# Kernel tuning notes

Measured on AMD Instinct MI355X. Metric: run time of the kernel, lower is better.

Reference implementation:

```python
import jax, jax.numpy as jnp
import numpy as np

B, C, H, W = 16, 128, 128, 128


def _gram(feat):
    # feat: [B, C, H, W] -> [B, C, HW]; gram: [B, C, C]
    f = feat.reshape(feat.shape[0], feat.shape[1], -1)
    return jnp.einsum('bcn,bdn->bcd', f, f)


def setup_inputs() -> dict:
    key = jax.random.key(0)
    k1, k2 = jax.random.split(key)
    feat = jax.random.normal(k1, (B, C, H, W), dtype=jnp.float32)
    feat_decod = jax.random.normal(k2, (B, C, H, W), dtype=jnp.float32)
    return {"feat": feat, "feat_decod": feat_decod}


def reference(feat, feat_decod):
    feat_size = feat.shape[2] * feat.shape[3]  # H*W
    feat_nb = feat.shape[1]                     # C
    gram_enc = _gram(feat)
    gram_dec = _gram(feat_decod)
    diff = gram_dec - gram_enc
    # per-sample scalar loss: [B]
    denom = 4.0 * feat_size * feat_size * feat_nb * feat_nb
    return jnp.sum(diff * diff, axis=(-2, -1)) / denom
```

## Files before the change

### kernel.cpp

```cpp
#include <hip/hip_runtime.h>
#include <hip/hip_bf16.h>


typedef __attribute__((ext_vector_type(8))) short short8;
typedef __attribute__((ext_vector_type(4))) float f32x4;

#define CC 128
#define NN 16384

__device__ __forceinline__ short f2bf(float x) {
    unsigned u = __builtin_bit_cast(unsigned, x);
    u += 0x7fffu + ((u >> 16) & 1u);
    return (short)(u >> 16);
}

__global__ __launch_bounds__(256, 4) void gram_partial_k(
    const float* __restrict__ f0, const float* __restrict__ f1,
    float* __restrict__ partials, int S, int Kc, int nst)
{
    __shared__ short lds[2][CC * 64];

    const int tid = threadIdx.x;
    const int bx  = blockIdx.x;
    const int g   = bx & 31;
    const int s   = bx >> 5;

    const float* src  = (g & 1) ? f1 : f0;
    const float* base = src + (size_t)(g >> 1) * ((size_t)CC * NN) + (size_t)s * Kc;

    const int srow = tid >> 3;
    const int scb  = tid & 7;
    const float* gp = base + (size_t)srow * NN + scb * 8;

    const int lane = tid & 63;
    const int w    = tid >> 6;
    const int m0   = (w & 1) * 64;
    const int n0   = (w >> 1) * 64;
    const int lr   = lane & 15;
    const int lk   = lane >> 4;

    const int rot = bx & (nst - 1);

    f32x4 acc[4][4];
    #pragma unroll
    for (int i = 0; i < 4; ++i)
        #pragma unroll
        for (int j = 0; j < 4; ++j)
            acc[i][j] = (f32x4){0.f, 0.f, 0.f, 0.f};

    float4 ra[4], rb[4];

    auto load_stage = [&](int st) {
        int sp = (st + rot) & (nst - 1);
        #pragma unroll
        for (int it = 0; it < 4; ++it) {
            const float* p = gp + (size_t)it * 32 * NN + (size_t)sp * 64;
            ra[it] = *(const float4*)p;
            rb[it] = *(const float4*)(p + 4);
        }
    };

    auto store_stage = [&](int buf) {
        #pragma unroll
        for (int it = 0; it < 4; ++it) {
            int r = srow + 32 * it;
            short8 v = { f2bf(ra[it].x), f2bf(ra[it].y), f2bf(ra[it].z), f2bf(ra[it].w),
                         f2bf(rb[it].x), f2bf(rb[it].y), f2bf(rb[it].z), f2bf(rb[it].w) };
            int phys = scb ^ (r & 7);
            *(short8*)&lds[buf][r * 64 + phys * 8] = v;
        }
    };

    auto compute = [&](int buf) {
        #pragma unroll
        for (int ks = 0; ks < 2; ++ks) {
            short8 af[4], bfr[4];
            int cb = ks * 4 + lk;
            #pragma unroll
            for (int i = 0; i < 4; ++i) {
                int r = m0 + i * 16 + lr;
                af[i] = *(const short8*)&lds[buf][r * 64 + ((cb ^ (r & 7)) * 8)];
            }
            #pragma unroll
            for (int i = 0; i < 4; ++i) {
                int r = n0 + i * 16 + lr;
                bfr[i] = *(const short8*)&lds[buf][r * 64 + ((cb ^ (r & 7)) * 8)];
            }
            #pragma unroll
            for (int mi = 0; mi < 4; ++mi)
                #pragma unroll
                for (int ni = 0; ni < 4; ++ni)
                    acc[mi][ni] = __builtin_amdgcn_mfma_f32_16x16x32_bf16(
                        af[mi], bfr[ni], acc[mi][ni], 0, 0, 0);
        }
    };

    load_stage(0);
    store_stage(0);
    __syncthreads();
    for (int st = 0; st < nst; ++st) {
        int cur = st & 1;
        bool more = (st + 1 < nst);
        if (more) load_stage(st + 1);
        compute(cur);
        if (more) store_stage(cur ^ 1);
        __syncthreads();
    }

    float* op = partials + ((size_t)g * S + s) * (CC * CC);
    #pragma unroll
    for (int mi = 0; mi < 4; ++mi)
        #pragma unroll
        for (int ni = 0; ni < 4; ++ni)
            #pragma unroll
            for (int i = 0; i < 4; ++i) {
                int row = m0 + mi * 16 + lk * 4 + i;
                int col = n0 + ni * 16 + lr;
                op[row * CC + col] = acc[mi][ni][i];
            }
}

__global__ __launch_bounds__(256) void reduce1_k(
    const float* __restrict__ partials, float* __restrict__ part2, int S)
{
    int b     = blockIdx.x >> 4;
    int chunk = blockIdx.x & 15;
    int t     = threadIdx.x;
    size_t e  = (size_t)chunk * 1024 + (size_t)t * 4;

    const f32x4* Pe = (const f32x4*)(partials + ((size_t)(2 * b) * S) * (CC * CC) + e);
    const f32x4* Pd = (const f32x4*)(partials + ((size_t)(2 * b + 1) * S) * (CC * CC) + e);
    const size_t stride = (size_t)CC * CC / 4;

    f32x4 ae = {0.f, 0.f, 0.f, 0.f}, ad = {0.f, 0.f, 0.f, 0.f};
    #pragma unroll 8
    for (int s2 = 0; s2 < S; ++s2) {
        ae += Pe[(size_t)s2 * stride];
        ad += Pd[(size_t)s2 * stride];
    }
    f32x4 d = ad - ae;
    float v = d[0] * d[0] + d[1] * d[1] + d[2] * d[2] + d[3] * d[3];
    #pragma unroll
    for (int off = 32; off > 0; off >>= 1) v += __shfl_down(v, off);
    __shared__ float wsum[4];
    if ((t & 63) == 0) wsum[t >> 6] = v;
    __syncthreads();
    if (t == 0) part2[b * 16 + chunk] = wsum[0] + wsum[1] + wsum[2] + wsum[3];
}

__global__ void reduce2_k(const float* __restrict__ part2, float* __restrict__ out)
{
    int b = blockIdx.x;
    int t = threadIdx.x;
    float v = (t < 16) ? part2[b * 16 + t] : 0.f;
    #pragma unroll
    for (int off = 8; off > 0; off >>= 1) v += __shfl_down(v, off);
    if (t == 0) out[b] = v * (1.0f / 17592186044416.0f);
}

extern "C" void kernel_launch(void* const* d_in, const int* in_sizes, int n_in,
                              void* d_out, int out_size, void* d_ws, size_t ws_size,
                              hipStream_t stream)
{
    const float* f0 = (const float*)d_in[0];
    const float* f1 = (const float*)d_in[1];
    float* out = (float*)d_out;

    const size_t perS = 32ull * CC * CC * 4;
    const size_t tail = 16 * 16 * 4;
    int S = 32;
    while (S > 1 && perS * (size_t)S + tail > ws_size) S >>= 1;
    int Kc  = NN / S;
    int nst = Kc / 64;

    float* partials = (float*)d_ws;
    float* part2    = (float*)((char*)d_ws + perS * (size_t)S);

    gram_partial_k<<<32 * S, 256, 0, stream>>>(f0, f1, partials, S, Kc, nst);
    reduce1_k<<<16 * 16, 256, 0, stream>>>(partials, part2, S);
    reduce2_k<<<16, 64, 0, stream>>>(part2, out);
}
```

Before: 299.1 us.

## Pre-pack inputs to swizzled bf16 tiles and stream them via global_load_lds

Adds a pack kernel that converts both fp32 feature tensors into bf16 stage tiles already laid out in the swizzled LDS format. The gram kernel then copies those tiles straight into LDS with global_load_lds, which removes the per-stage register conversion and the LDS store work. The split count drops from 32 to 16 and occupancy hints change. The cost is an extra pass that writes and re-reads 128 MB of packed data. A fallback direct kernel runs when the workspace is too small.

```diff
diff --git a/kernel.cpp b/kernel.cpp
--- a/kernel.cpp
+++ b/kernel.cpp
@@ -1,8 +1,8 @@
 #include <hip/hip_runtime.h>
-#include <hip/hip_bf16.h>
 
 
 typedef __attribute__((ext_vector_type(8))) short short8;
+typedef __attribute__((ext_vector_type(4))) short short4v;
 typedef __attribute__((ext_vector_type(4))) float f32x4;
 
 #define CC 128
@@ -14,9 +14,44 @@
     return (short)(u >> 16);
 }
 
-__global__ __launch_bounds__(256, 4) void gram_partial_k(
+__global__ __launch_bounds__(512, 2) void pack_k(
     const float* __restrict__ f0, const float* __restrict__ f1,
-    float* __restrict__ partials, int S, int Kc, int nst)
+    short* __restrict__ packed)
+{
+    const int bx = blockIdx.x;
+    const int rg = bx & 3;
+    const int kr = (bx >> 2) & 3;
+    const int g  = bx >> 4;
+
+    const float* src  = (g & 1) ? f1 : f0;
+    const float* base = src + (size_t)(g >> 1) * ((size_t)CC * NN);
+
+    const int t    = threadIdx.x;
+    const int lane = t & 63;
+    const int w    = t >> 6;
+
+    const int c  = (lane & 15) >> 1;
+    const int hf = lane & 1;
+    const int sl = lane >> 4;
+
+    char* pg = (char*)packed + (size_t)g * 256 * 16384;
+
+    for (int rr = 0; rr < 4; ++rr) {
+        const int row = rg * 32 + w * 4 + rr;
+        const float* rp = base + (size_t)row * NN + kr * 4096 + lane * 4;
+        const size_t rowoff = (size_t)row * 128 + (size_t)(((c ^ (row & 7)) * 16) + hf * 8);
+        #pragma unroll 4
+        for (int ii = 0; ii < 16; ++ii) {
+            f32x4 v = __builtin_nontemporal_load((const f32x4*)(rp + (size_t)ii * 256));
+            short4v b = { f2bf(v[0]), f2bf(v[1]), f2bf(v[2]), f2bf(v[3]) };
+            const int ST = kr * 64 + ii * 4 + sl;
+            *(short4v*)(pg + (size_t)ST * 16384 + rowoff) = b;
+        }
+    }
+}
+
+__global__ __launch_bounds__(256, 2) void gram_packed_k(
+    const short* __restrict__ packed, float* __restrict__ partials, int S, int nst)
 {
     __shared__ short lds[2][CC * 64];
 
@@ -25,12 +60,7 @@
     const int g   = bx & 31;
     const int s   = bx >> 5;
 
-    const float* src  = (g & 1) ? f1 : f0;
-    const float* base = src + (size_t)(g >> 1) * ((size_t)CC * NN) + (size_t)s * Kc;
-
-    const int srow = tid >> 3;
-    const int scb  = tid & 7;
-    const float* gp = base + (size_t)srow * NN + scb * 8;
+    const char* pk = (const char*)packed + (size_t)(g * 256 + s * nst) * 16384;
 
     const int lane = tid & 63;
     const int w    = tid >> 6;
@@ -39,8 +69,6 @@
     const int lr   = lane & 15;
     const int lk   = lane >> 4;
 
-    const int rot = bx & (nst - 1);
-
     f32x4 acc[4][4];
     #pragma unroll
     for (int i = 0; i < 4; ++i)
@@ -48,13 +76,101 @@
         for (int j = 0; j < 4; ++j)
             acc[i][j] = (f32x4){0.f, 0.f, 0.f, 0.f};
 
+    auto issue = [&](int j, int buf) {
+        const char* sb = pk + (size_t)j * 16384;
+        #pragma unroll
+        for (int i = 0; i < 4; ++i) {
+            const int off = (w * 4 + i) * 1024;
+            __builtin_amdgcn_global_load_lds(
+                (const __attribute__((address_space(1))) void*)(sb + off + lane * 16),
+                (__attribute__((address_space(3))) void*)((char*)&lds[buf][0] + off),
+                16, 0, 0);
+        }
+    };
+
+    auto compute = [&](int buf) {
+        #pragma unroll
+        for (int ks = 0; ks < 2; ++ks) {
+            short8 af[4], bfr[4];
+            const int cb = ks * 4 + lk;
+            #pragma unroll
+            for (int i = 0; i < 4; ++i) {
+                int r = m0 + i * 16 + lr;
+                af[i] = *(const short8*)&lds[buf][r * 64 + ((cb ^ (r & 7)) * 8)];
+            }
+            #pragma unroll
+            for (int i = 0; i < 4; ++i) {
+                int r = n0 + i * 16 + lr;
+                bfr[i] = *(const short8*)&lds[buf][r * 64 + ((cb ^ (r & 7)) * 8)];
+            }
+            #pragma unroll
+            for (int mi = 0; mi < 4; ++mi)
+                #pragma unroll
+                for (int ni = 0; ni < 4; ++ni)
+                    acc[mi][ni] = __builtin_amdgcn_mfma_f32_16x16x32_bf16(
+                        af[mi], bfr[ni], acc[mi][ni], 0, 0, 0);
+        }
+    };
+
+    issue(0, 0);
+    __syncthreads();
+    for (int j = 0; j < nst; ++j) {
+        if (j + 1 < nst) issue(j + 1, (j + 1) & 1);
+        compute(j & 1);
+        __syncthreads();
+    }
+
+    float* op = partials + ((size_t)g * S + s) * (CC * CC);
+    #pragma unroll
+    for (int mi = 0; mi < 4; ++mi)
+        #pragma unroll
+        for (int ni = 0; ni < 4; ++ni)
+            #pragma unroll
+            for (int i = 0; i < 4; ++i) {
+                int row = m0 + mi * 16 + lk * 4 + i;
+                int col = n0 + ni * 16 + lr;
+                op[row * CC + col] = acc[mi][ni][i];
+            }
+}
+
+__global__ __launch_bounds__(256, 2) void gram_direct_k(
+    const float* __restrict__ f0, const float* __restrict__ f1,
+    float* __restrict__ partials, int S, int Kc, int nst)
+{
+    __shared__ short lds[2][CC * 64];
+
+    const int tid = threadIdx.x;
+    const int bx  = blockIdx.x;
+    const int g   = bx & 31;
+    const int s   = bx >> 5;
+
+    const float* src  = (g & 1) ? f1 : f0;
+    const float* base = src + (size_t)(g >> 1) * ((size_t)CC * NN) + (size_t)s * Kc;
+
+    const int srow = tid >> 3;
+    const int scb  = tid & 7;
+    const float* gp = base + (size_t)srow * NN + scb * 8;
+
+    const int lane = tid & 63;
+    const int w    = tid >> 6;
+    const int m0   = (w & 1) * 64;
+    const int n0   = (w >> 1) * 64;
+    const int lr   = lane & 15;
+    const int lk   = lane >> 4;
+
+    f32x4 acc[4][4];
+    #pragma unroll
+    for (int i = 0; i < 4; ++i)
+        #pragma unroll
+        for (int j = 0; j < 4; ++j)
+            acc[i][j] = (f32x4){0.f, 0.f, 0.f, 0.f};
+
     float4 ra[4], rb[4];
 
     auto load_stage = [&](int st) {
-        int sp = (st + rot) & (nst - 1);
         #pragma unroll
         for (int it = 0; it < 4; ++it) {
-            const float* p = gp + (size_t)it * 32 * NN + (size_t)sp * 64;
+            const float* p = gp + (size_t)it * 32 * NN + (size_t)st * 64;
             ra[it] = *(const float4*)p;
             rb[it] = *(const float4*)(p + 4);
         }
@@ -166,17 +282,27 @@
     const float* f1 = (const float*)d_in[1];
     float* out = (float*)d_out;
 
+    const size_t packed_bytes = 32ull * 256 * 16384;
     const size_t perS = 32ull * CC * CC * 4;
     const size_t tail = 16 * 16 * 4;
-    int S = 32;
-    while (S > 1 && perS * (size_t)S + tail > ws_size) S >>= 1;
-    int Kc  = NN / S;
-    int nst = Kc / 64;
-
-    float* partials = (float*)d_ws;
-    float* part2    = (float*)((char*)d_ws + perS * (size_t)S);
-
-    gram_partial_k<<<32 * S, 256, 0, stream>>>(f0, f1, partials, S, Kc, nst);
-    reduce1_k<<<16 * 16, 256, 0, stream>>>(partials, part2, S);
-    reduce2_k<<<16, 64, 0, stream>>>(part2, out);
-}
+
+    if (ws_size >= packed_bytes + perS * 16 + tail) {
+        short* packed   = (short*)d_ws;
+        float* partials = (float*)((char*)d_ws + packed_bytes);
+        float* part2    = (float*)((char*)d_ws + packed_bytes + perS * 16);
+        pack_k<<<512, 512, 0, stream>>>(f0, f1, packed);
+        gram_packed_k<<<32 * 16, 256, 0, stream>>>(packed, partials, 16, 16);
+        reduce1_k<<<16 * 16, 256, 0, stream>>>(partials, part2, 16);
+        reduce2_k<<<16, 64, 0, stream>>>(part2, out);
+    } else {
+        int S = 16;
+        while (S > 1 && perS * (size_t)S + tail > ws_size) S >>= 1;
+        int Kc  = NN / S;
+        int nst = Kc / 64;
+        float* partials = (float*)d_ws;
+        float* part2    = (float*)((char*)d_ws + perS * (size_t)S);
+        gram_direct_k<<<32 * S, 256, 0, stream>>>(f0, f1, partials, S, Kc, nst);
+        reduce1_k<<<16 * 16, 256, 0, stream>>>(partials, part2, S);
+        reduce2_k<<<16, 64, 0, stream>>>(part2, out);
+    }
+}
```

Result: slower. 318.6 us (+6.5%).

## Use 512-thread blocks with large single-buffer K tiles and fewer K splits

Applied to the files above, without the earlier changes.

Restructures the gram kernel to 512-thread blocks that stage a 128x512 bf16 tile into shared memory, with each wave computing a 64x32 sub-tile. The K-split count drops from 32 to 8, which shrinks the partial buffers and the reduction traffic. The double-buffered register prefetch and stage rotation are removed, so global loads no longer overlap MFMA work inside a block. Only 256 blocks are launched, which may underfill the GPU, and the 128KB shared tile limits occupancy.

```diff
diff --git a/kernel.cpp b/kernel.cpp
--- a/kernel.cpp
+++ b/kernel.cpp
@@ -1,5 +1,4 @@
 #include <hip/hip_runtime.h>
-#include <hip/hip_bf16.h>
 
 
 typedef __attribute__((ext_vector_type(8))) short short8;
@@ -7,6 +6,7 @@
 
 #define CC 128
 #define NN 16384
+#define BK 512
 
 __device__ __forceinline__ short f2bf(float x) {
     unsigned u = __builtin_bit_cast(unsigned, x);
@@ -14,11 +14,11 @@
     return (short)(u >> 16);
 }
 
-__global__ __launch_bounds__(256, 4) void gram_partial_k(
+__global__ __launch_bounds__(512, 2) void gram_k(
     const float* __restrict__ f0, const float* __restrict__ f1,
     float* __restrict__ partials, int S, int Kc, int nst)
 {
-    __shared__ short lds[2][CC * 64];
+    __shared__ short lds[CC * BK];
 
     const int tid = threadIdx.x;
     const int bx  = blockIdx.x;
@@ -28,82 +28,65 @@
     const float* src  = (g & 1) ? f1 : f0;
     const float* base = src + (size_t)(g >> 1) * ((size_t)CC * NN) + (size_t)s * Kc;
 
-    const int srow = tid >> 3;
-    const int scb  = tid & 7;
-    const float* gp = base + (size_t)srow * NN + scb * 8;
-
     const int lane = tid & 63;
     const int w    = tid >> 6;
     const int m0   = (w & 1) * 64;
-    const int n0   = (w >> 1) * 64;
+    const int n0   = (w >> 1) * 32;
     const int lr   = lane & 15;
     const int lk   = lane >> 4;
 
-    const int rot = bx & (nst - 1);
-
-    f32x4 acc[4][4];
+    f32x4 acc[4][2];
     #pragma unroll
     for (int i = 0; i < 4; ++i)
         #pragma unroll
-        for (int j = 0; j < 4; ++j)
+        for (int j = 0; j < 2; ++j)
             acc[i][j] = (f32x4){0.f, 0.f, 0.f, 0.f};
 
-    float4 ra[4], rb[4];
+    for (int st = 0; st < nst; ++st) {
+        const float* sb = base + (size_t)st * BK;
 
-    auto load_stage = [&](int st) {
-        int sp = (st + rot) & (nst - 1);
         #pragma unroll
-        for (int it = 0; it < 4; ++it) {
-            const float* p = gp + (size_t)it * 32 * NN + (size_t)sp * 64;
-            ra[it] = *(const float4*)p;
-            rb[it] = *(const float4*)(p + 4);
+        for (int grp = 0; grp < 4; ++grp) {
+            float4 va[4], vb[4];
+            #pragma unroll
+            for (int q = 0; q < 4; ++q) {
+                const int r = w * 16 + grp * 4 + q;
+                const float* rp = sb + (size_t)r * NN + lane * 8;
+                va[q] = *(const float4*)rp;
+                vb[q] = *(const float4*)(rp + 4);
+            }
+            #pragma unroll
+            for (int q = 0; q < 4; ++q) {
+                const int r = w * 16 + grp * 4 + q;
+                short8 v = { f2bf(va[q].x), f2bf(va[q].y), f2bf(va[q].z), f2bf(va[q].w),
+                             f2bf(vb[q].x), f2bf(vb[q].y), f2bf(vb[q].z), f2bf(vb[q].w) };
+                const int phys = lane ^ (r & 7);
+                *(short8*)&lds[r * BK + phys * 8] = v;
+            }
         }
-    };
+        __syncthreads();
 
-    auto store_stage = [&](int buf) {
         #pragma unroll
-        for (int it = 0; it < 4; ++it) {
-            int r = srow + 32 * it;
-            short8 v = { f2bf(ra[it].x), f2bf(ra[it].y), f2bf(ra[it].z), f2bf(ra[it].w),
-                         f2bf(rb[it].x), f2bf(rb[it].y), f2bf(rb[it].z), f2bf(rb[it].w) };
-            int phys = scb ^ (r & 7);
-            *(short8*)&lds[buf][r * 64 + phys * 8] = v;
-        }
-    };
-
-    auto compute = [&](int buf) {
-        #pragma unroll
-        for (int ks = 0; ks < 2; ++ks) {
-            short8 af[4], bfr[4];
-            int cb = ks * 4 + lk;
+        for (int ks = 0; ks < BK / 32; ++ks) {
+            short8 af[4], bf2[2];
+            const int c = ks * 4 + lk;
             #pragma unroll
             for (int i = 0; i < 4; ++i) {
-                int r = m0 + i * 16 + lr;
-                af[i] = *(const short8*)&lds[buf][r * 64 + ((cb ^ (r & 7)) * 8)];
+                const int r = m0 + i * 16 + lr;
+                af[i] = *(const short8*)&lds[r * BK + ((c ^ (r & 7)) * 8)];
             }
             #pragma unroll
-            for (int i = 0; i < 4; ++i) {
-                int r = n0 + i * 16 + lr;
-                bfr[i] = *(const short8*)&lds[buf][r * 64 + ((cb ^ (r & 7)) * 8)];
+            for (int j = 0; j < 2; ++j) {
+                const int r = n0 + j * 16 + lr;
+                bf2[j] = *(const short8*)&lds[r * BK + ((c ^ (r & 7)) * 8)];
             }
             #pragma unroll
             for (int mi = 0; mi < 4; ++mi)
                 #pragma unroll
-                for (int ni = 0; ni < 4; ++ni)
+                for (int ni = 0; ni < 2; ++ni)
                     acc[mi][ni] = __builtin_amdgcn_mfma_f32_16x16x32_bf16(
-                        af[mi], bfr[ni], acc[mi][ni], 0, 0, 0);
+                        af[mi], bf2[ni], acc[mi][ni], 0, 0, 0);
         }
-    };
-
-    load_stage(0);
-    store_stage(0);
-    __syncthreads();
-    for (int st = 0; st < nst; ++st) {
-        int cur = st & 1;
-        bool more = (st + 1 < nst);
-        if (more) load_stage(st + 1);
-        compute(cur);
-        if (more) store_stage(cur ^ 1);
         __syncthreads();
     }
 
@@ -111,11 +94,11 @@
     #pragma unroll
     for (int mi = 0; mi < 4; ++mi)
         #pragma unroll
-        for (int ni = 0; ni < 4; ++ni)
+        for (int ni = 0; ni < 2; ++ni)
             #pragma unroll
             for (int i = 0; i < 4; ++i) {
-                int row = m0 + mi * 16 + lk * 4 + i;
-                int col = n0 + ni * 16 + lr;
+                const int row = m0 + mi * 16 + lk * 4 + i;
+                const int col = n0 + ni * 16 + lr;
                 op[row * CC + col] = acc[mi][ni][i];
             }
 }
@@ -168,15 +151,15 @@
 
     const size_t perS = 32ull * CC * CC * 4;
     const size_t tail = 16 * 16 * 4;
-    int S = 32;
+    int S = 8;
     while (S > 1 && perS * (size_t)S + tail > ws_size) S >>= 1;
     int Kc  = NN / S;
-    int nst = Kc / 64;
+    int nst = Kc / BK;
 
     float* partials = (float*)d_ws;
     float* part2    = (float*)((char*)d_ws + perS * (size_t)S);
 
-    gram_partial_k<<<32 * S, 256, 0, stream>>>(f0, f1, partials, S, Kc, nst);
+    gram_k<<<32 * S, 512, 0, stream>>>(f0, f1, partials, S, Kc, nst);
     reduce1_k<<<16 * 16, 256, 0, stream>>>(partials, part2, S);
     reduce2_k<<<16, 64, 0, stream>>>(part2, out);
 }
```

Measured after the change: 295.3 us. No clear change (-1.3%).
